# Kernel tuning notes

Hardware: AMD Instinct MI355X
Metric: run time of the kernel (lower is better)

Reference implementation:

```python
import jax, jax.numpy as jnp
import numpy as np

N_POINTS = 2_000_000
N_BATCH = 8


def cart2polar(xyz):
    rho = jnp.sqrt(xyz[:, 0] ** 2 + xyz[:, 1] ** 2)
    phi = jnp.arctan2(xyz[:, 1], xyz[:, 0])
    return jnp.stack((rho, phi, xyz[:, 2]), axis=1)


def setup_inputs() -> dict:
    key = jax.random.key(0)
    k1, k2, k3, k4 = jax.random.split(key, 4)
    xy = jax.random.uniform(k1, (N_POINTS, 2), minval=-50.0, maxval=50.0)
    z = jax.random.uniform(k2, (N_POINTS, 1), minval=-4.0, maxval=2.0)
    inten = jax.random.uniform(k3, (N_POINTS, 1))
    points = jnp.concatenate([xy, z, inten], axis=1)  # [N, 4]
    batch_idx = jnp.sort(jax.random.randint(k4, (N_POINTS,), 0, N_BATCH)).astype(jnp.int32)
    coors_range_xyz = jnp.array([[0.0, 50.0], [-np.pi, np.pi], [-4.0, 2.0]], dtype=jnp.float32)
    spatial_shape = np.array([480, 360, 32])  # static
    scale_list = np.array([2, 4, 1])          # module appends 1; static
    return dict(points=points, batch_idx=batch_idx,
                coors_range_xyz=coors_range_xyz,
                spatial_shape=spatial_shape, scale_list=scale_list)


def _unique_rows(bxyz, dims):
    # Encode [b, gx, gy, gz] rows into a single int32 key (max 8*480*360*32 ~ 44M).
    key = ((bxyz[:, 0] * dims[0] + bxyz[:, 1]) * dims[1] + bxyz[:, 2]) * dims[2] + bxyz[:, 3]
    order = jnp.argsort(key)
    sk = key[order]
    flags = jnp.concatenate([jnp.ones((1,), bool), sk[1:] != sk[:-1]])
    rank = jnp.cumsum(flags.astype(jnp.int32)) - 1          # unique-id per sorted row
    inv = jnp.zeros_like(rank).at[order].set(rank)           # inverse map, like torch.unique
    # first occurrence of each unique row (all rows with same rank are identical)
    unq = jnp.zeros_like(bxyz).at[rank].set(bxyz[order])     # padded to [N, 4]
    num_unique = rank[-1] + 1
    return unq, inv, num_unique


def reference(points, batch_idx, coors_range_xyz, spatial_shape, scale_list):
    pc = points[:, :3]
    xyz_pol = cart2polar(pc)
    lo = coors_range_xyz[:, 0]
    hi = coors_range_xyz[:, 1]
    crop = hi - lo
    ss_np = np.asarray(spatial_shape)
    outs = []
    for scale in [int(s) for s in np.asarray(scale_list)]:
        cells = jnp.asarray(np.ceil(ss_np / scale) - 1.0, dtype=xyz_pol.dtype)
        grid = jnp.floor((jnp.clip(xyz_pol, lo, hi) - lo) / crop * cells).astype(jnp.int32)
        bxyz = jnp.concatenate([batch_idx[:, None].astype(jnp.int32), grid], axis=1)  # [N,4]
        dims = np.ceil(ss_np / scale).astype(np.int64)
        unq, inv, num = _unique_rows(bxyz, dims)
        # reorder unique coords as [b, z, y, x], cast int32 (torch: unq[:, [0,3,2,1]])
        coors = jnp.concatenate([unq[:, 0:1], unq[:, 3:4], unq[:, 2:3], unq[:, 1:2]], axis=1).astype(jnp.int32)
        outs.extend([bxyz, inv, coors, num])
    return tuple(outs)
```

## Files before the change

kernel.cpp:

```cpp
#include <hip/hip_runtime.h>
#include <cstdint>

#define DI __device__ __forceinline__

constexpr int NPTS       = 2000000;
constexpr int STRIDE_OUT = 18000001;
constexpr int OFF_INV    = 8000000;
constexpr int OFF_COORS  = 10000000;
constexpr int OFF_NUM    = 18000000;

constexpr int R2W  = 172800;
constexpr int R4W  = 21600;
constexpr int R1W  = 1382400;
constexpr int RW0  = 0;
constexpr int RW1  = R2W;
constexpr int RW2  = R2W + R4W;
constexpr int WTOT = R2W + R4W + R1W;
constexpr int NB1  = (WTOT + 1023) / 1024;
constexpr int J2   = 8;
constexpr int J1   = 4;
constexpr int S1W  = 28800;
constexpr int S1BITS = S1W * 32;

constexpr int NBLK_INVU  = (NPTS + 1023) / 1024;
constexpr int NBLK_INVUP = ((NBLK_INVU + 7) / 8) * 8;
constexpr int IVQ        = NBLK_INVUP / 8;
constexpr int NBLK_COORS = (WTOT + 255) / 256;
constexpr int NBLK_TAIL  = (3 * NPTS + 255) / 256;

DI float fmul_s(float a, float b){ float r; asm("v_mul_f32 %0, %1, %2" : "=v"(r) : "v"(a), "v"(b)); return r; }
DI float fadd_s(float a, float b){ float r; asm("v_add_f32 %0, %1, %2" : "=v"(r) : "v"(a), "v"(b)); return r; }

__global__ __launch_bounds__(256) void pass_keys(const float4* __restrict__ pts,
                                                 const int* __restrict__ batch, int n,
                                                 int* __restrict__ keys,
                                                 int* __restrict__ bstart,
                                                 int* __restrict__ out) {
  int i = blockIdx.x * 256 + threadIdx.x;
  if (i >= n) return;
  float4 p = pts[i];
  int bi = batch[i];
  const float PI_F     = 3.14159265358979323846f;
  const float TWO_PI_F = 6.28318530717958647692f;
  float rho = sqrtf(fadd_s(fmul_s(p.x, p.x), fmul_s(p.y, p.y)));
  float phi = atan2f(p.y, p.x);
  float tr = (fminf(fmaxf(rho, 0.0f), 50.0f) - 0.0f) / 50.0f;
  float tp = (fminf(fmaxf(phi, -PI_F), PI_F) + PI_F) / TWO_PI_F;
  float tz = (fminf(fmaxf(p.z, -4.0f), 2.0f) + 4.0f) / 6.0f;
  constexpr float C0[3] = {239.f, 119.f, 479.f};
  constexpr float C1[3] = {179.f,  89.f, 359.f};
  constexpr float C2[3] = { 15.f,   7.f,  31.f};
  constexpr int   D0[3] = {240, 120, 480};
  constexpr int   D1[3] = {180,  90, 360};
  constexpr int   D2[3] = { 16,   8,  32};
  #pragma unroll
  for (int s = 0; s < 3; ++s) {
    int a0 = (int)floorf(tr * C0[s]);
    int a1 = (int)floorf(tp * C1[s]);
    int a2 = (int)floorf(tz * C2[s]);
    keys[s * n + i] = ((bi * D0[s] + a0) * D1[s] + a1) * D2[s] + a2;
    *reinterpret_cast<int4*>(out + s * STRIDE_OUT + (size_t)i * 4) = make_int4(bi, a0, a1, a2);
  }
  if (i == 0) {
    #pragma unroll 1
    for (int k = 0; k <= bi; ++k) bstart[k] = 0;
  }
  int bnext = (i + 1 < n) ? batch[i + 1] : 8;
  #pragma unroll 1
  for (int k = bi + 1; k <= bnext; ++k) bstart[k] = i + 1;
}

__global__ __launch_bounds__(1024) void hist_all(const int* __restrict__ bstart,
                                                 const int* __restrict__ keys, int n,
                                                 uint32_t* __restrict__ rep2s,
                                                 uint32_t* __restrict__ rep4s,
                                                 uint32_t* __restrict__ rep1s) {
  alignas(16) __shared__ uint32_t bmA[S1W];
  alignas(16) __shared__ uint32_t bmB[2700];
  int t = threadIdx.x;
  int pb = blockIdx.x;
  if (pb < 64) {
    int bv = pb & 7, j = pb >> 3;
    for (int w = t * 4; w < 21600; w += 4096) *reinterpret_cast<uint4*>(bmA + w) = make_uint4(0,0,0,0);
    for (int w = t; w < 2700; w += 1024) bmB[w] = 0;
    __syncthreads();
    int lo = bstart[bv];
    int hi = bstart[bv + 1];
    int sz = hi - lo;
    int s = lo + (int)((long long)sz * j / J2);
    int e = lo + (int)((long long)sz * (j + 1) / J2);
    const int* k0 = keys;
    const int* k1 = keys + n;
    int b2 = bv * 691200;
    int b4 = bv * 86400;
    int i = s + t;
    for (; i < e - 3072; i += 4096) {
      int a0 = k0[i], a1 = k0[i + 1024], a2 = k0[i + 2048], a3 = k0[i + 3072];
      int c0 = k1[i], c1 = k1[i + 1024], c2 = k1[i + 2048], c3 = k1[i + 3072];
      int x0 = a0 - b2, x1 = a1 - b2, x2 = a2 - b2, x3 = a3 - b2;
      int y0 = c0 - b4, y1 = c1 - b4, y2 = c2 - b4, y3 = c3 - b4;
      atomicOr(&bmA[x0 >> 5], 1u << (x0 & 31));
      atomicOr(&bmA[x1 >> 5], 1u << (x1 & 31));
      atomicOr(&bmA[x2 >> 5], 1u << (x2 & 31));
      atomicOr(&bmA[x3 >> 5], 1u << (x3 & 31));
      atomicOr(&bmB[y0 >> 5], 1u << (y0 & 31));
      atomicOr(&bmB[y1 >> 5], 1u << (y1 & 31));
      atomicOr(&bmB[y2 >> 5], 1u << (y2 & 31));
      atomicOr(&bmB[y3 >> 5], 1u << (y3 & 31));
    }
    for (; i < e; i += 1024) {
      int ink2 = k0[i] - b2;
      int ink4 = k1[i] - b4;
      atomicOr(&bmA[ink2 >> 5], 1u << (ink2 & 31));
      atomicOr(&bmB[ink4 >> 5], 1u << (ink4 & 31));
    }
    __syncthreads();
    uint32_t* d2 = rep2s + (size_t)j * R2W + bv * 21600;
    uint32_t* d4 = rep4s + (size_t)j * R4W + bv * 2700;
    for (int w = t * 4; w < 21600; w += 4096) *reinterpret_cast<uint4*>(d2 + w) = *reinterpret_cast<uint4*>(bmA + w);
    for (int w = t * 4; w < 2700; w += 4096) *reinterpret_cast<uint4*>(d4 + w) = *reinterpret_cast<uint4*>(bmB + w);
  } else {
    int bv = pb & 7;
    int id = (pb - 64) >> 3;
    int j = id / 6, r = id - j * 6;
    int slice = bv * 6 + r;
    for (int w = t * 4; w < S1W; w += 4096) *reinterpret_cast<uint4*>(bmA + w) = make_uint4(0,0,0,0);
    __syncthreads();
    int lo = bstart[bv];
    int hi = bstart[bv + 1];
    int sz = hi - lo;
    int s = lo + (int)((long long)sz * j / J1);
    int e = lo + (int)((long long)sz * (j + 1) / J1);
    const int* k2 = keys + 2 * n;
    int base = bv * 5529600 + r * S1BITS;
    int i = s + t;
    for (; i < e - 3072; i += 4096) {
      int r0 = k2[i] - base, r1 = k2[i + 1024] - base;
      int r2 = k2[i + 2048] - base, r3 = k2[i + 3072] - base;
      if ((unsigned)r0 < (unsigned)S1BITS) atomicOr(&bmA[r0 >> 5], 1u << (r0 & 31));
      if ((unsigned)r1 < (unsigned)S1BITS) atomicOr(&bmA[r1 >> 5], 1u << (r1 & 31));
      if ((unsigned)r2 < (unsigned)S1BITS) atomicOr(&bmA[r2 >> 5], 1u << (r2 & 31));
      if ((unsigned)r3 < (unsigned)S1BITS) atomicOr(&bmA[r3 >> 5], 1u << (r3 & 31));
    }
    for (; i < e; i += 1024) {
      int rel = k2[i] - base;
      if ((unsigned)rel < (unsigned)S1BITS) atomicOr(&bmA[rel >> 5], 1u << (rel & 31));
    }
    __syncthreads();
    uint32_t* d = rep1s + (size_t)j * R1W + (size_t)slice * S1W;
    for (int w = t * 4; w < S1W; w += 4096) *reinterpret_cast<uint4*>(d + w) = *reinterpret_cast<uint4*>(bmA + w);
  }
}

DI uint4 merged_words(int base, const uint32_t* __restrict__ rep2s,
                      const uint32_t* __restrict__ rep4s,
                      const uint32_t* __restrict__ rep1s) {
  uint4 acc = make_uint4(0, 0, 0, 0);
  if (base < RW1) {
    #pragma unroll
    for (int c = 0; c < J2; ++c) {
      uint4 w = *reinterpret_cast<const uint4*>(rep2s + (size_t)c * R2W + base);
      acc.x |= w.x; acc.y |= w.y; acc.z |= w.z; acc.w |= w.w;
    }
  } else if (base < RW2) {
    int l = base - RW1;
    #pragma unroll
    for (int c = 0; c < J2; ++c) {
      uint4 w = *reinterpret_cast<const uint4*>(rep4s + (size_t)c * R4W + l);
      acc.x |= w.x; acc.y |= w.y; acc.z |= w.z; acc.w |= w.w;
    }
  } else {
    int l = base - RW2;
    #pragma unroll
    for (int c = 0; c < J1; ++c) {
      uint4 w = *reinterpret_cast<const uint4*>(rep1s + (size_t)c * R1W + l);
      acc.x |= w.x; acc.y |= w.y; acc.z |= w.z; acc.w |= w.w;
    }
  }
  return acc;
}

__global__ __launch_bounds__(256) void scanA(const uint32_t* __restrict__ rep2s,
                                             const uint32_t* __restrict__ rep4s,
                                             const uint32_t* __restrict__ rep1s,
                                             uint32_t* __restrict__ bits,
                                             uint32_t* __restrict__ blockSums) {
  __shared__ uint32_t lds[256];
  int t = threadIdx.x;
  int base = blockIdx.x * 1024 + t * 4;
  uint32_t s = 0;
  if (base < WTOT) {
    uint4 m = merged_words(base, rep2s, rep4s, rep1s);
    *reinterpret_cast<uint4*>(bits + base) = m;
    s = __popc(m.x) + __popc(m.y) + __popc(m.z) + __popc(m.w);
  }
  lds[t] = s; __syncthreads();
  for (int off = 128; off > 0; off >>= 1) { if (t < off) lds[t] += lds[t + off]; __syncthreads(); }
  if (t == 0) blockSums[blockIdx.x] = lds[0];
}

__global__ __launch_bounds__(256) void scanC(const uint32_t* __restrict__ bits,
                                             const uint32_t* __restrict__ blockSums,
                                             uint2* __restrict__ pairs) {
  __shared__ uint32_t lds[256];
  int t = threadIdx.x;
  uint32_t bs = 0;
  for (int k = t; k < (int)blockIdx.x; k += 256) bs += blockSums[k];
  lds[t] = bs; __syncthreads();
  for (int off = 128; off > 0; off >>= 1) { if (t < off) lds[t] += lds[t + off]; __syncthreads(); }
  uint32_t blockBase = lds[0];
  __syncthreads();
  int base = blockIdx.x * 1024 + t * 4;
  uint32_t b[4] = {0,0,0,0}; uint32_t c[4]; uint32_t sum = 0;
  if (base < WTOT) {
    uint4 w = *reinterpret_cast<const uint4*>(bits + base);
    b[0] = w.x; b[1] = w.y; b[2] = w.z; b[3] = w.w;
  }
  #pragma unroll
  for (int k = 0; k < 4; ++k) { c[k] = __popc(b[k]); sum += c[k]; }
  lds[t] = sum; __syncthreads();
  for (int off = 1; off < 256; off <<= 1) {
    uint32_t x = (t >= off) ? lds[t - off] : 0u; __syncthreads();
    lds[t] += x; __syncthreads();
  }
  uint32_t excl = lds[t] - sum + blockBase;
  if (base < WTOT) {
    #pragma unroll
    for (int k = 0; k < 4; ++k) { pairs[base + k] = make_uint2(b[k], excl); excl += c[k]; }
  }
}

template <int S>
DI int4 decode_key(int key) {
  constexpr int D0[3] = {240, 120, 480};
  constexpr int D1[3] = {180,  90, 360};
  constexpr int D2[3] = { 16,   8,  32};
  int a2 = key & (D2[S] - 1);
  int r  = key / D2[S];
  int q  = r / D1[S];
  int a1 = r - q * D1[S];
  int b  = q / D0[S];
  int a0 = q - b * D0[S];
  return make_int4(b, a0, a1, a2);
}

template <int S>
DI void coors_word(int wi_local, uint32_t bits, uint32_t rank, int* __restrict__ coors) {
  int keybase = wi_local * 32;
  while (bits) {
    int j = __builtin_ctz(bits);
    bits &= bits - 1;
    int4 d = decode_key<S>(keybase + j);
    *reinterpret_cast<int4*>(coors + (size_t)rank * 4) = make_int4(d.x, d.w, d.z, d.y);
    ++rank;
  }
}

__global__ __launch_bounds__(256) void epilogue(int n, const uint2* __restrict__ pairs,
                                                const int* __restrict__ keys,
                                                int* __restrict__ out) {
  int b = blockIdx.x;
  int t = threadIdx.x;
  if (b < NBLK_INVUP) {
    int lv = (b & 7) * IVQ + (b >> 3);
    if (lv >= NBLK_INVU) return;
    int i0 = lv * 1024 + t;
    uint32_t subs1 = pairs[RW1].y;
    uint32_t subs2 = pairs[RW2].y;
    int kv[3][4];
    bool ok[4];
    #pragma unroll
    for (int u = 0; u < 4; ++u) {
      int i = i0 + u * 256;
      ok[u] = (i < n);
      int ii = ok[u] ? i : 0;
      kv[0][u] = keys[ii];
      kv[1][u] = keys[n + ii];
      kv[2][u] = keys[2 * n + ii];
    }
    uint2 pr[3][4];
    #pragma unroll
    for (int u = 0; u < 4; ++u) {
      pr[0][u] = pairs[RW0 + (kv[0][u] >> 5)];
      pr[1][u] = pairs[RW1 + (kv[1][u] >> 5)];
      pr[2][u] = pairs[RW2 + (kv[2][u] >> 5)];
    }
    #pragma unroll
    for (int u = 0; u < 4; ++u) {
      if (!ok[u]) continue;
      int i = i0 + u * 256;
      out[0 * STRIDE_OUT + OFF_INV + i] =
          (int)(pr[0][u].y + __popc(pr[0][u].x & ((1u << (kv[0][u] & 31)) - 1u)));
      out[1 * STRIDE_OUT + OFF_INV + i] =
          (int)(pr[1][u].y - subs1 + __popc(pr[1][u].x & ((1u << (kv[1][u] & 31)) - 1u)));
      out[2 * STRIDE_OUT + OFF_INV + i] =
          (int)(pr[2][u].y - subs2 + __popc(pr[2][u].x & ((1u << (kv[2][u] & 31)) - 1u)));
    }
  } else if (b < NBLK_INVUP + NBLK_COORS) {
    int wi = (b - NBLK_INVUP) * 256 + t;
    if (wi >= WTOT) return;
    uint2 pr = pairs[wi];
    if (!pr.x) return;
    if (wi < RW1)      coors_word<0>(wi,       pr.x, pr.y,                 out + 0 * STRIDE_OUT + OFF_COORS);
    else if (wi < RW2) coors_word<1>(wi - RW1, pr.x, pr.y - pairs[RW1].y,  out + 1 * STRIDE_OUT + OFF_COORS);
    else               coors_word<2>(wi - RW2, pr.x, pr.y - pairs[RW2].y,  out + 2 * STRIDE_OUT + OFF_COORS);
  } else {
    int idx = (b - NBLK_INVUP - NBLK_COORS) * 256 + t;
    if (idx >= 3 * n) return;
    int s = 0, i = idx;
    if (i >= 2 * n)  { s = 2; i -= 2 * n; }
    else if (i >= n) { s = 1; i -= n; }
    uint2 last = pairs[WTOT - 1];
    uint32_t total = last.y + (uint32_t)__popc(last.x);
    uint32_t lo = (s == 0) ? 0u : pairs[(s == 1) ? RW1 : RW2].y;
    uint32_t hi = (s == 0) ? pairs[RW1].y : (s == 1) ? pairs[RW2].y : total;
    uint32_t num = hi - lo;
    if (i == 0) out[s * STRIDE_OUT + OFF_NUM] = (int)num;
    if ((uint32_t)i >= num)
      *reinterpret_cast<int4*>(out + s * STRIDE_OUT + OFF_COORS + (size_t)i * 4) = make_int4(0, 0, 0, 0);
  }
}

extern "C" void kernel_launch(void* const* d_in, const int* in_sizes, int n_in,
                              void* d_out, int out_size, void* d_ws, size_t ws_size,
                              hipStream_t stream) {
  const float4* pts   = (const float4*)d_in[0];
  const int*    batch = (const int*)d_in[1];
  int n = in_sizes[1];
  int* out = (int*)d_out;

  uint32_t* rep2s     = (uint32_t*)d_ws;
  uint32_t* rep4s     = rep2s + (size_t)J2 * R2W;
  uint32_t* rep1s     = rep4s + (size_t)J2 * R4W;
  uint32_t* bits      = rep1s + (size_t)J1 * R1W;
  uint2*    pairs     = (uint2*)(bits + WTOT);
  uint32_t* blockSums = (uint32_t*)(pairs + WTOT);
  int*      bstart    = (int*)(blockSums + NB1);
  int*      keys      = (int*)(bstart + 16);

  int nblk = (n + 255) / 256;
  pass_keys<<<nblk, 256, 0, stream>>>(pts, batch, n, keys, bstart, out);
  hist_all<<<256, 1024, 0, stream>>>(bstart, keys, n, rep2s, rep4s, rep1s);
  scanA<<<NB1, 256, 0, stream>>>(rep2s, rep4s, rep1s, bits, blockSums);
  scanC<<<NB1, 256, 0, stream>>>(bits, blockSums, pairs);
  epilogue<<<NBLK_INVUP + NBLK_COORS + NBLK_TAIL, 256, 0, stream>>>(n, pairs, keys, out);
}
```

Baseline: 333.8 us.

## Fuse bitmap histogram into key pass with global atomicOr

Drops the separate LDS-bitmap histogram kernel, its per-chunk replica bitmaps and the merge step in scanA. Instead, the key kernel sets occupancy bits directly in one global bitmap using atomicOr, after a memset of that bitmap. This removes a kernel launch, the replica writes and the replica reads. In exchange it issues 6M global atomics, which may contend on shared words for the coarse scales.

```diff
diff --git a/kernel.cpp b/kernel.cpp
--- a/kernel.cpp
+++ b/kernel.cpp
@@ -17,10 +17,6 @@
 constexpr int RW2  = R2W + R4W;
 constexpr int WTOT = R2W + R4W + R1W;
 constexpr int NB1  = (WTOT + 1023) / 1024;
-constexpr int J2   = 8;
-constexpr int J1   = 4;
-constexpr int S1W  = 28800;
-constexpr int S1BITS = S1W * 32;
 
 constexpr int NBLK_INVU  = (NPTS + 1023) / 1024;
 constexpr int NBLK_INVUP = ((NBLK_INVU + 7) / 8) * 8;
@@ -31,10 +27,10 @@
 DI float fmul_s(float a, float b){ float r; asm("v_mul_f32 %0, %1, %2" : "=v"(r) : "v"(a), "v"(b)); return r; }
 DI float fadd_s(float a, float b){ float r; asm("v_add_f32 %0, %1, %2" : "=v"(r) : "v"(a), "v"(b)); return r; }
 
-__global__ __launch_bounds__(256) void pass_keys(const float4* __restrict__ pts,
+__global__ __launch_bounds__(256) void keys_hist(const float4* __restrict__ pts,
                                                  const int* __restrict__ batch, int n,
                                                  int* __restrict__ keys,
-                                                 int* __restrict__ bstart,
+                                                 uint32_t* __restrict__ bits,
                                                  int* __restrict__ out) {
   int i = blockIdx.x * 256 + threadIdx.x;
   if (i >= n) return;
@@ -53,145 +49,27 @@
   constexpr int   D0[3] = {240, 120, 480};
   constexpr int   D1[3] = {180,  90, 360};
   constexpr int   D2[3] = { 16,   8,  32};
+  constexpr int   RW[3] = {RW0, RW1, RW2};
   #pragma unroll
   for (int s = 0; s < 3; ++s) {
     int a0 = (int)floorf(tr * C0[s]);
     int a1 = (int)floorf(tp * C1[s]);
     int a2 = (int)floorf(tz * C2[s]);
-    keys[s * n + i] = ((bi * D0[s] + a0) * D1[s] + a1) * D2[s] + a2;
+    int key = ((bi * D0[s] + a0) * D1[s] + a1) * D2[s] + a2;
+    keys[s * n + i] = key;
     *reinterpret_cast<int4*>(out + s * STRIDE_OUT + (size_t)i * 4) = make_int4(bi, a0, a1, a2);
-  }
-  if (i == 0) {
-    #pragma unroll 1
-    for (int k = 0; k <= bi; ++k) bstart[k] = 0;
-  }
-  int bnext = (i + 1 < n) ? batch[i + 1] : 8;
-  #pragma unroll 1
-  for (int k = bi + 1; k <= bnext; ++k) bstart[k] = i + 1;
-}
-
-__global__ __launch_bounds__(1024) void hist_all(const int* __restrict__ bstart,
-                                                 const int* __restrict__ keys, int n,
-                                                 uint32_t* __restrict__ rep2s,
-                                                 uint32_t* __restrict__ rep4s,
-                                                 uint32_t* __restrict__ rep1s) {
-  alignas(16) __shared__ uint32_t bmA[S1W];
-  alignas(16) __shared__ uint32_t bmB[2700];
-  int t = threadIdx.x;
-  int pb = blockIdx.x;
-  if (pb < 64) {
-    int bv = pb & 7, j = pb >> 3;
-    for (int w = t * 4; w < 21600; w += 4096) *reinterpret_cast<uint4*>(bmA + w) = make_uint4(0,0,0,0);
-    for (int w = t; w < 2700; w += 1024) bmB[w] = 0;
-    __syncthreads();
-    int lo = bstart[bv];
-    int hi = bstart[bv + 1];
-    int sz = hi - lo;
-    int s = lo + (int)((long long)sz * j / J2);
-    int e = lo + (int)((long long)sz * (j + 1) / J2);
-    const int* k0 = keys;
-    const int* k1 = keys + n;
-    int b2 = bv * 691200;
-    int b4 = bv * 86400;
-    int i = s + t;
-    for (; i < e - 3072; i += 4096) {
-      int a0 = k0[i], a1 = k0[i + 1024], a2 = k0[i + 2048], a3 = k0[i + 3072];
-      int c0 = k1[i], c1 = k1[i + 1024], c2 = k1[i + 2048], c3 = k1[i + 3072];
-      int x0 = a0 - b2, x1 = a1 - b2, x2 = a2 - b2, x3 = a3 - b2;
-      int y0 = c0 - b4, y1 = c1 - b4, y2 = c2 - b4, y3 = c3 - b4;
-      atomicOr(&bmA[x0 >> 5], 1u << (x0 & 31));
-      atomicOr(&bmA[x1 >> 5], 1u << (x1 & 31));
-      atomicOr(&bmA[x2 >> 5], 1u << (x2 & 31));
-      atomicOr(&bmA[x3 >> 5], 1u << (x3 & 31));
-      atomicOr(&bmB[y0 >> 5], 1u << (y0 & 31));
-      atomicOr(&bmB[y1 >> 5], 1u << (y1 & 31));
-      atomicOr(&bmB[y2 >> 5], 1u << (y2 & 31));
-      atomicOr(&bmB[y3 >> 5], 1u << (y3 & 31));
-    }
-    for (; i < e; i += 1024) {
-      int ink2 = k0[i] - b2;
-      int ink4 = k1[i] - b4;
-      atomicOr(&bmA[ink2 >> 5], 1u << (ink2 & 31));
-      atomicOr(&bmB[ink4 >> 5], 1u << (ink4 & 31));
-    }
-    __syncthreads();
-    uint32_t* d2 = rep2s + (size_t)j * R2W + bv * 21600;
-    uint32_t* d4 = rep4s + (size_t)j * R4W + bv * 2700;
-    for (int w = t * 4; w < 21600; w += 4096) *reinterpret_cast<uint4*>(d2 + w) = *reinterpret_cast<uint4*>(bmA + w);
-    for (int w = t * 4; w < 2700; w += 4096) *reinterpret_cast<uint4*>(d4 + w) = *reinterpret_cast<uint4*>(bmB + w);
-  } else {
-    int bv = pb & 7;
-    int id = (pb - 64) >> 3;
-    int j = id / 6, r = id - j * 6;
-    int slice = bv * 6 + r;
-    for (int w = t * 4; w < S1W; w += 4096) *reinterpret_cast<uint4*>(bmA + w) = make_uint4(0,0,0,0);
-    __syncthreads();
-    int lo = bstart[bv];
-    int hi = bstart[bv + 1];
-    int sz = hi - lo;
-    int s = lo + (int)((long long)sz * j / J1);
-    int e = lo + (int)((long long)sz * (j + 1) / J1);
-    const int* k2 = keys + 2 * n;
-    int base = bv * 5529600 + r * S1BITS;
-    int i = s + t;
-    for (; i < e - 3072; i += 4096) {
-      int r0 = k2[i] - base, r1 = k2[i + 1024] - base;
-      int r2 = k2[i + 2048] - base, r3 = k2[i + 3072] - base;
-      if ((unsigned)r0 < (unsigned)S1BITS) atomicOr(&bmA[r0 >> 5], 1u << (r0 & 31));
-      if ((unsigned)r1 < (unsigned)S1BITS) atomicOr(&bmA[r1 >> 5], 1u << (r1 & 31));
-      if ((unsigned)r2 < (unsigned)S1BITS) atomicOr(&bmA[r2 >> 5], 1u << (r2 & 31));
-      if ((unsigned)r3 < (unsigned)S1BITS) atomicOr(&bmA[r3 >> 5], 1u << (r3 & 31));
-    }
-    for (; i < e; i += 1024) {
-      int rel = k2[i] - base;
-      if ((unsigned)rel < (unsigned)S1BITS) atomicOr(&bmA[rel >> 5], 1u << (rel & 31));
-    }
-    __syncthreads();
-    uint32_t* d = rep1s + (size_t)j * R1W + (size_t)slice * S1W;
-    for (int w = t * 4; w < S1W; w += 4096) *reinterpret_cast<uint4*>(d + w) = *reinterpret_cast<uint4*>(bmA + w);
-  }
-}
-
-DI uint4 merged_words(int base, const uint32_t* __restrict__ rep2s,
-                      const uint32_t* __restrict__ rep4s,
-                      const uint32_t* __restrict__ rep1s) {
-  uint4 acc = make_uint4(0, 0, 0, 0);
-  if (base < RW1) {
-    #pragma unroll
-    for (int c = 0; c < J2; ++c) {
-      uint4 w = *reinterpret_cast<const uint4*>(rep2s + (size_t)c * R2W + base);
-      acc.x |= w.x; acc.y |= w.y; acc.z |= w.z; acc.w |= w.w;
-    }
-  } else if (base < RW2) {
-    int l = base - RW1;
-    #pragma unroll
-    for (int c = 0; c < J2; ++c) {
-      uint4 w = *reinterpret_cast<const uint4*>(rep4s + (size_t)c * R4W + l);
-      acc.x |= w.x; acc.y |= w.y; acc.z |= w.z; acc.w |= w.w;
-    }
-  } else {
-    int l = base - RW2;
-    #pragma unroll
-    for (int c = 0; c < J1; ++c) {
-      uint4 w = *reinterpret_cast<const uint4*>(rep1s + (size_t)c * R1W + l);
-      acc.x |= w.x; acc.y |= w.y; acc.z |= w.z; acc.w |= w.w;
-    }
-  }
-  return acc;
-}
-
-__global__ __launch_bounds__(256) void scanA(const uint32_t* __restrict__ rep2s,
-                                             const uint32_t* __restrict__ rep4s,
-                                             const uint32_t* __restrict__ rep1s,
-                                             uint32_t* __restrict__ bits,
+    atomicOr(&bits[RW[s] + (key >> 5)], 1u << (key & 31));
+  }
+}
+
+__global__ __launch_bounds__(256) void scanA(const uint32_t* __restrict__ bits,
                                              uint32_t* __restrict__ blockSums) {
   __shared__ uint32_t lds[256];
   int t = threadIdx.x;
   int base = blockIdx.x * 1024 + t * 4;
   uint32_t s = 0;
   if (base < WTOT) {
-    uint4 m = merged_words(base, rep2s, rep4s, rep1s);
-    *reinterpret_cast<uint4*>(bits + base) = m;
+    uint4 m = *reinterpret_cast<const uint4*>(bits + base);
     s = __popc(m.x) + __popc(m.y) + __popc(m.z) + __popc(m.w);
   }
   lds[t] = s; __syncthreads();
@@ -329,19 +207,15 @@
   int n = in_sizes[1];
   int* out = (int*)d_out;
 
-  uint32_t* rep2s     = (uint32_t*)d_ws;
-  uint32_t* rep4s     = rep2s + (size_t)J2 * R2W;
-  uint32_t* rep1s     = rep4s + (size_t)J2 * R4W;
-  uint32_t* bits      = rep1s + (size_t)J1 * R1W;
+  uint32_t* bits      = (uint32_t*)d_ws;
   uint2*    pairs     = (uint2*)(bits + WTOT);
   uint32_t* blockSums = (uint32_t*)(pairs + WTOT);
-  int*      bstart    = (int*)(blockSums + NB1);
-  int*      keys      = (int*)(bstart + 16);
-
+  int*      keys      = (int*)(blockSums + NB1 + 16);
+
+  hipMemsetAsync(bits, 0, (size_t)WTOT * 4, stream);
   int nblk = (n + 255) / 256;
-  pass_keys<<<nblk, 256, 0, stream>>>(pts, batch, n, keys, bstart, out);
-  hist_all<<<256, 1024, 0, stream>>>(bstart, keys, n, rep2s, rep4s, rep1s);
-  scanA<<<NB1, 256, 0, stream>>>(rep2s, rep4s, rep1s, bits, blockSums);
+  keys_hist<<<nblk, 256, 0, stream>>>(pts, batch, n, keys, bits, out);
+  scanA<<<NB1, 256, 0, stream>>>(bits, blockSums);
   scanC<<<NB1, 256, 0, stream>>>(bits, blockSums, pairs);
   epilogue<<<NBLK_INVUP + NBLK_COORS + NBLK_TAIL, 256, 0, stream>>>(n, pairs, keys, out);
 }
```

Result: slower. 942.9 us (+182.5%).
